# Performance work log

Measured on AMD Instinct MI355X. Metric: run time of the kernel, lower is better.

## Reference

```python
import jax, jax.numpy as jnp
import numpy as np

NUM_CATS = 5
EPS = 1e-6


def setup_inputs() -> dict:
    key = jax.random.key(0)
    k1, k2, k3, k4 = jax.random.split(key, 4)
    B, C, H, W = 64, 3, 256, 256
    restored = jax.random.normal(k1, (B, C, H, W), dtype=jnp.float32)
    clean_patch_1 = jax.random.normal(k2, (B, C, H, W), dtype=jnp.float32)
    un = jax.random.uniform(k3, (B, C, H, W), dtype=jnp.float32)
    de_id = jax.random.randint(k4, (B,), 0, NUM_CATS)
    return {"restored": restored, "clean_patch_1": clean_patch_1,
            "de_id": de_id, "un": un}


def _loss(restored, clean, un, de_id):
    B, C, H, W = restored.shape
    E = C * H * W  # elements per sample
    dt = restored.dtype

    onehot = (de_id[:, None] == jnp.arange(NUM_CATS)[None, :])  # [B,5] bool
    m = onehot.astype(dt)                                        # [B,5]
    counts = onehot.sum(0)                                       # [5] int
    nonempty = counts > 0
    safe_counts = jnp.maximum(counts, 1).astype(dt)              # avoid 0-div

    # Per-category mean uncertainty map: un_map[c] = mean_{i: de_id[i]=c} un[i] + eps
    un_sum = jnp.einsum('bk,bchw->kchw', m, un)                  # [5,C,H,W]
    un_map = un_sum / safe_counts[:, None, None, None] + EPS     # [5,C,H,W]
    s = 1.0 / un_map                                             # [5,C,H,W]

    # Per-sample scaled L1 (s gathered by each sample's category)
    absdiff = jnp.abs(clean - restored)                          # [B,C,H,W]
    scaled_sum_per_sample = (absdiff * s[de_id]).sum(axis=(1, 2, 3))  # [B]
    abs_sum_per_sample = absdiff.sum(axis=(1, 2, 3))                  # [B]

    cat_scaled_sum = jnp.einsum('bk,b->k', m, scaled_sum_per_sample)  # [5]
    cat_abs_sum = jnp.einsum('bk,b->k', m, abs_sum_per_sample)        # [5]

    # NOTE: the original code never clears un_hq_list/un_lq_list between
    # categories, so the L1 at category c is the mean over ALL samples from
    # categories 0..c (each scaled by its OWN category's s). Replicate that
    # via cumulative sums/counts over the category axis.
    cum_scaled = jnp.cumsum(cat_scaled_sum)                      # [5]
    cum_elems = jnp.cumsum(counts).astype(dt) * E                # [5]
    cum_l1 = cum_scaled / jnp.maximum(cum_elems, 1.0)            # [5]

    old_loss = jnp.where(nonempty, cat_abs_sum / (safe_counts * E), 0.0)
    un_num = un_map.mean(axis=(1, 2, 3))                         # [5]
    bn = jnp.where(nonempty, 2.0 * jnp.log(un_num), 0.0)
    unc_l1 = jnp.where(nonempty, cum_l1, 0.0)

    cat_losses = unc_l1 + bn                                     # [5]
    num = nonempty.sum().astype(dt)
    total = cat_losses.sum() / num
    return total, cat_losses, old_loss, bn, unc_l1


def reference(restored, clean_patch_1, de_id, un):
    return _loss(restored, clean_patch_1, un, de_id)
```

## Files before the change

### kernel.cpp

```cpp
#include <hip/hip_runtime.h>
#include <math.h>

#define NCAT  5
#define BATCH 64
#define ELEMS 196608
#define NBLK  768
#define TPB   256
#define GRP   8
#define EPSV  1e-6f

__global__ __launch_bounds__(TPB) void accum_kernel(
    const float* __restrict__ restored,
    const float* __restrict__ clean,
    const int*   __restrict__ de_id,
    const float* __restrict__ un,
    float*       __restrict__ partials)
{
    __shared__ int   sh_de[BATCH];
    __shared__ float sh_inv[NCAT];
    __shared__ float sred[TPB / 64][3 * NCAT];

    const int tid = threadIdx.x;

    if (tid < 64) {
        int k = de_id[tid];
        sh_de[tid] = k;
        #pragma unroll
        for (int j = 0; j < NCAT; ++j) {
            unsigned long long m = __ballot(k == j);
            if (tid == j) {
                int c = __popcll(m);
                sh_inv[j] = 1.0f / (float)(c > 0 ? c : 1);
            }
        }
    }
    __syncthreads();

    const int p = blockIdx.x * TPB + tid;
    const float* rp = restored + p;
    const float* cp = clean + p;
    const float* up = un + p;

    float un_s[NCAT] = {0.f, 0.f, 0.f, 0.f, 0.f};
    float ad_s[NCAT] = {0.f, 0.f, 0.f, 0.f, 0.f};

    float ub[2][GRP], cb[2][GRP], rb[2][GRP];

    #pragma unroll
    for (int i = 0; i < GRP; ++i) {
        const size_t off = (size_t)i * ELEMS;
        ub[0][i] = up[off];
        cb[0][i] = cp[off];
        rb[0][i] = rp[off];
    }

    #pragma unroll
    for (int g = 0; g < BATCH / GRP; ++g) {
        const int cur = g & 1;
        const int nxt = cur ^ 1;
        if (g < BATCH / GRP - 1) {
            #pragma unroll
            for (int i = 0; i < GRP; ++i) {
                const size_t off = (size_t)((g + 1) * GRP + i) * ELEMS;
                ub[nxt][i] = up[off];
                cb[nxt][i] = cp[off];
                rb[nxt][i] = rp[off];
            }
        }
        #pragma unroll
        for (int i = 0; i < GRP; ++i) {
            float u  = ub[cur][i];
            float ad = fabsf(cb[cur][i] - rb[cur][i]);
            int   k  = sh_de[g * GRP + i];
            #pragma unroll
            for (int j = 0; j < NCAT; ++j) {
                float m = (k == j) ? 1.0f : 0.0f;
                un_s[j] = fmaf(m, u,  un_s[j]);
                ad_s[j] = fmaf(m, ad, ad_s[j]);
            }
        }
    }

    float vals[3 * NCAT];
    #pragma unroll
    for (int j = 0; j < NCAT; ++j) {
        float um = fmaf(un_s[j], sh_inv[j], EPSV);
        vals[j]            = ad_s[j] / um;
        vals[NCAT + j]     = ad_s[j];
        vals[2 * NCAT + j] = un_s[j];
    }

    #pragma unroll
    for (int i = 0; i < 3 * NCAT; ++i) {
        float v = vals[i];
        #pragma unroll
        for (int off = 32; off >= 1; off >>= 1)
            v += __shfl_down(v, off, 64);
        vals[i] = v;
    }

    const int wave = tid >> 6;
    const int lane = tid & 63;
    if (lane == 0) {
        #pragma unroll
        for (int i = 0; i < 3 * NCAT; ++i) sred[wave][i] = vals[i];
    }
    __syncthreads();

    if (tid < 3 * NCAT) {
        float v = sred[0][tid] + sred[1][tid] + sred[2][tid] + sred[3][tid];
        partials[tid * NBLK + blockIdx.x] = v;
    }
}

__global__ __launch_bounds__(256) void epilogue_kernel(
    const int*   __restrict__ de_id,
    const float* __restrict__ partials,
    float*       __restrict__ out)
{
    __shared__ int   sh_cnt[NCAT];
    __shared__ float sh_acc[3 * NCAT];

    const int tid = threadIdx.x;

    if (tid < 64) {
        int k = de_id[tid];
        #pragma unroll
        for (int j = 0; j < NCAT; ++j) {
            unsigned long long m = __ballot(k == j);
            if (tid == j) sh_cnt[j] = __popcll(m);
        }
    }

    if (tid < 240) {
        const int row    = tid >> 4;
        const int lane16 = tid & 15;
        float v = 0.f;
        #pragma unroll 4
        for (int k = 0; k < NBLK / 16; ++k)
            v += partials[row * NBLK + lane16 + (k << 4)];
        v += __shfl_down(v, 8, 16);
        v += __shfl_down(v, 4, 16);
        v += __shfl_down(v, 2, 16);
        v += __shfl_down(v, 1, 16);
        if (lane16 == 0) sh_acc[row] = v;
    }
    __syncthreads();

    if (tid == 0) {
        const float Ef = (float)ELEMS;
        float cum_s = 0.f;
        long  cum_c = 0;
        float total = 0.f;
        int   num   = 0;

        float cat_losses[NCAT], old_loss[NCAT], bn[NCAT], unc_l1[NCAT];

        for (int j = 0; j < NCAT; ++j) {
            cum_s += sh_acc[j];
            cum_c += sh_cnt[j];
            float cum_elems = (float)cum_c * Ef;
            float cum_l1    = cum_s / fmaxf(cum_elems, 1.0f);

            bool  ne   = sh_cnt[j] > 0;
            float safe = (float)(ne ? sh_cnt[j] : 1);

            old_loss[j]  = ne ? sh_acc[NCAT + j] / (safe * Ef) : 0.f;
            float un_num = sh_acc[2 * NCAT + j] / (safe * Ef) + EPSV;
            bn[j]        = ne ? 2.0f * logf(un_num) : 0.f;
            unc_l1[j]    = ne ? cum_l1 : 0.f;
            cat_losses[j] = unc_l1[j] + bn[j];
            total += cat_losses[j];
            num   += ne ? 1 : 0;
        }
        total /= (float)num;

        out[0] = total;
        for (int j = 0; j < NCAT; ++j) {
            out[1 + j]  = cat_losses[j];
            out[6 + j]  = old_loss[j];
            out[11 + j] = bn[j];
            out[16 + j] = unc_l1[j];
        }
    }
}

extern "C" void kernel_launch(void* const* d_in, const int* in_sizes, int n_in,
                              void* d_out, int out_size, void* d_ws, size_t ws_size,
                              hipStream_t stream) {
    (void)in_sizes; (void)n_in; (void)out_size; (void)ws_size;
    const float* restored = (const float*)d_in[0];
    const float* clean    = (const float*)d_in[1];
    const int*   de_id    = (const int*)d_in[2];
    const float* un       = (const float*)d_in[3];
    float* out      = (float*)d_out;
    float* partials = (float*)d_ws;

    accum_kernel<<<NBLK, TPB, 0, stream>>>(restored, clean, de_id, un, partials);
    epilogue_kernel<<<1, 256, 0, stream>>>(de_id, partials, out);
}
```

Baseline: 174.2 us.

## Split batch across waves and shrink per-block positions to raise parallelism

Each block now covers 64 positions with four waves, each accumulating a 16-sample slice of the batch. Per-position category sums are then combined through shared memory before the uncertainty division. This quadruples the grid and cuts the serial load chain per thread, raising memory-level parallelism. The cost is extra LDS traffic and barriers, and a partials buffer four times larger that the epilogue, now run with 1024 threads, has to reduce.

```diff
diff --git a/kernel.cpp b/kernel.cpp
--- a/kernel.cpp
+++ b/kernel.cpp
@@ -4,8 +4,10 @@
 #define NCAT  5
 #define BATCH 64
 #define ELEMS 196608
-#define NBLK  768
+#define POSB  64
+#define NBLK  (ELEMS / POSB)
 #define TPB   256
+#define CHUNK 16
 #define GRP   8
 #define EPSV  1e-6f
 
@@ -18,11 +20,13 @@
 {
     __shared__ int   sh_de[BATCH];
     __shared__ float sh_inv[NCAT];
-    __shared__ float sred[TPB / 64][3 * NCAT];
-
-    const int tid = threadIdx.x;
-
-    if (tid < 64) {
+    __shared__ float sbuf[2][2 * NCAT][POSB];
+
+    const int tid  = threadIdx.x;
+    const int lane = tid & 63;
+    const int wave = tid >> 6;
+
+    if (tid < BATCH) {
         int k = de_id[tid];
         sh_de[tid] = k;
         #pragma unroll
@@ -36,10 +40,11 @@
     }
     __syncthreads();
 
-    const int p = blockIdx.x * TPB + tid;
-    const float* rp = restored + p;
-    const float* cp = clean + p;
-    const float* up = un + p;
+    const size_t base = (size_t)(wave * CHUNK) * ELEMS
+                      + (size_t)blockIdx.x * POSB + lane;
+    const float* rp = restored + base;
+    const float* cp = clean + base;
+    const float* up = un + base;
 
     float un_s[NCAT] = {0.f, 0.f, 0.f, 0.f, 0.f};
     float ad_s[NCAT] = {0.f, 0.f, 0.f, 0.f, 0.f};
@@ -55,10 +60,10 @@
     }
 
     #pragma unroll
-    for (int g = 0; g < BATCH / GRP; ++g) {
+    for (int g = 0; g < CHUNK / GRP; ++g) {
         const int cur = g & 1;
         const int nxt = cur ^ 1;
-        if (g < BATCH / GRP - 1) {
+        if (g < CHUNK / GRP - 1) {
             #pragma unroll
             for (int i = 0; i < GRP; ++i) {
                 const size_t off = (size_t)((g + 1) * GRP + i) * ELEMS;
@@ -71,7 +76,7 @@
         for (int i = 0; i < GRP; ++i) {
             float u  = ub[cur][i];
             float ad = fabsf(cb[cur][i] - rb[cur][i]);
-            int   k  = sh_de[g * GRP + i];
+            int   k  = sh_de[wave * CHUNK + g * GRP + i];
             #pragma unroll
             for (int j = 0; j < NCAT; ++j) {
                 float m = (k == j) ? 1.0f : 0.0f;
@@ -81,39 +86,64 @@
         }
     }
 
-    float vals[3 * NCAT];
-    #pragma unroll
-    for (int j = 0; j < NCAT; ++j) {
-        float um = fmaf(un_s[j], sh_inv[j], EPSV);
-        vals[j]            = ad_s[j] / um;
-        vals[NCAT + j]     = ad_s[j];
-        vals[2 * NCAT + j] = un_s[j];
-    }
-
-    #pragma unroll
-    for (int i = 0; i < 3 * NCAT; ++i) {
-        float v = vals[i];
-        #pragma unroll
-        for (int off = 32; off >= 1; off >>= 1)
-            v += __shfl_down(v, off, 64);
-        vals[i] = v;
-    }
-
-    const int wave = tid >> 6;
-    const int lane = tid & 63;
-    if (lane == 0) {
-        #pragma unroll
-        for (int i = 0; i < 3 * NCAT; ++i) sred[wave][i] = vals[i];
-    }
-    __syncthreads();
-
-    if (tid < 3 * NCAT) {
-        float v = sred[0][tid] + sred[1][tid] + sred[2][tid] + sred[3][tid];
-        partials[tid * NBLK + blockIdx.x] = v;
+    if (wave >= 2) {
+        #pragma unroll
+        for (int j = 0; j < NCAT; ++j) {
+            sbuf[wave - 2][j][lane]        = un_s[j];
+            sbuf[wave - 2][NCAT + j][lane] = ad_s[j];
+        }
+    }
+    __syncthreads();
+    if (wave < 2) {
+        #pragma unroll
+        for (int j = 0; j < NCAT; ++j) {
+            un_s[j] += sbuf[wave][j][lane];
+            ad_s[j] += sbuf[wave][NCAT + j][lane];
+        }
+    }
+    __syncthreads();
+    if (wave == 1) {
+        #pragma unroll
+        for (int j = 0; j < NCAT; ++j) {
+            sbuf[0][j][lane]        = un_s[j];
+            sbuf[0][NCAT + j][lane] = ad_s[j];
+        }
+    }
+    __syncthreads();
+    if (wave == 0) {
+        #pragma unroll
+        for (int j = 0; j < NCAT; ++j) {
+            un_s[j] += sbuf[0][j][lane];
+            ad_s[j] += sbuf[0][NCAT + j][lane];
+        }
+
+        float vals[3 * NCAT];
+        #pragma unroll
+        for (int j = 0; j < NCAT; ++j) {
+            float um = fmaf(un_s[j], sh_inv[j], EPSV);
+            vals[j]            = ad_s[j] / um;
+            vals[NCAT + j]     = ad_s[j];
+            vals[2 * NCAT + j] = un_s[j];
+        }
+
+        #pragma unroll
+        for (int i = 0; i < 3 * NCAT; ++i) {
+            float v = vals[i];
+            #pragma unroll
+            for (int off = 32; off >= 1; off >>= 1)
+                v += __shfl_down(v, off, 64);
+            vals[i] = v;
+        }
+
+        if (lane == 0) {
+            #pragma unroll
+            for (int i = 0; i < 3 * NCAT; ++i)
+                partials[i * NBLK + blockIdx.x] = vals[i];
+        }
     }
 }
 
-__global__ __launch_bounds__(256) void epilogue_kernel(
+__global__ __launch_bounds__(1024) void epilogue_kernel(
     const int*   __restrict__ de_id,
     const float* __restrict__ partials,
     float*       __restrict__ out)
@@ -121,7 +151,9 @@
     __shared__ int   sh_cnt[NCAT];
     __shared__ float sh_acc[3 * NCAT];
 
-    const int tid = threadIdx.x;
+    const int tid  = threadIdx.x;
+    const int lane = tid & 63;
+    const int row  = tid >> 6;
 
     if (tid < 64) {
         int k = de_id[tid];
@@ -132,18 +164,15 @@
         }
     }
 
-    if (tid < 240) {
-        const int row    = tid >> 4;
-        const int lane16 = tid & 15;
+    if (row < 3 * NCAT) {
         float v = 0.f;
-        #pragma unroll 4
-        for (int k = 0; k < NBLK / 16; ++k)
-            v += partials[row * NBLK + lane16 + (k << 4)];
-        v += __shfl_down(v, 8, 16);
-        v += __shfl_down(v, 4, 16);
-        v += __shfl_down(v, 2, 16);
-        v += __shfl_down(v, 1, 16);
-        if (lane16 == 0) sh_acc[row] = v;
+        #pragma unroll 8
+        for (int k = 0; k < NBLK / 64; ++k)
+            v += partials[row * NBLK + lane + (k << 6)];
+        #pragma unroll
+        for (int off = 32; off >= 1; off >>= 1)
+            v += __shfl_down(v, off, 64);
+        if (lane == 0) sh_acc[row] = v;
     }
     __syncthreads();
 
@@ -197,5 +226,5 @@
     float* partials = (float*)d_ws;
 
     accum_kernel<<<NBLK, TPB, 0, stream>>>(restored, clean, de_id, un, partials);
-    epilogue_kernel<<<1, 256, 0, stream>>>(de_id, partials, out);
+    epilogue_kernel<<<1, 1024, 0, stream>>>(de_id, partials, out);
 }
```

New measurement: 176.1 us. No clear change (+1.1%).
